# Kernel tuning notes

Hardware: AMD Instinct MI355X
Metric: run time of the kernel (lower is better)

## Reference

```python
import jax, jax.numpy as jnp
import numpy as np

B, L, D, V = 512, 128, 512, 100000

def setup_inputs() -> dict:
    key = jax.random.key(0)
    ks = jax.random.split(key, 8)
    return {
        "t1s": jax.random.randint(ks[0], (B,), 0, V),
        "t2s": jax.random.randint(ks[1], (B,), 0, V),
        "t1_contexts": jax.random.randint(ks[2], (B, L), 0, V),
        "t2_contexts": jax.random.randint(ks[3], (B, L), 0, V),
        "embed_table": jax.random.normal(ks[4], (V, D), dtype=jnp.float32),
        "att_mat": jax.random.normal(ks[5], (D, D), dtype=jnp.float32) * (6.0 / (D + D)) ** 0.5,
        "w_pred": jax.random.normal(ks[6], (D, 1), dtype=jnp.float32) * 0.02,
        "b_pred": jnp.zeros((1,), dtype=jnp.float32),
    }

def _frob_normalize(x):
    # torch.norm(mat, p=2) is the Frobenius norm of the whole (L, D) matrix
    n = jnp.sqrt(jnp.sum(x * x, axis=(1, 2), keepdims=True))
    return x / n

def reference(t1s, t2s, t1_contexts, t2_contexts, embed_table, att_mat, w_pred, b_pred):
    # dropout is identity in eval mode; t1s/t2s embeddings are unused in the
    # 'dynamic' branch (dead code in the original forward).
    A = _frob_normalize(embed_table[t1_contexts])  # (B, L, D)
    Bm = _frob_normalize(embed_table[t2_contexts])  # (B, L, D)
    # batched bilinear attention: tanh(A @ att_mat @ B^T)
    S = jnp.tanh(jnp.einsum('bld,de,bme->blm', A, att_mat, Bm))  # (B, L, L)
    rows = jax.nn.softmax(jnp.mean(S, axis=2), axis=1)  # (B, L)
    cols = jax.nn.softmax(jnp.mean(S, axis=1), axis=1)  # (B, L)
    newA = jnp.einsum('bld,bl->bd', A, rows)   # (B, D)
    newB = jnp.einsum('bld,bl->bd', Bm, cols)  # (B, D)
    logits = ((newA * newB) @ w_pred + b_pred).reshape(-1)  # (B,)
    return logits, S
```

## Files before the change

### kernel.cpp

```cpp
#include <hip/hip_runtime.h>
#include <hip/hip_bf16.h>
#include <stdint.h>

#define NB 512
#define NL 128
#define ND 512

typedef __bf16 bf16;
typedef __bf16 bf16x8 __attribute__((ext_vector_type(8)));
typedef float  f32x4  __attribute__((ext_vector_type(4)));

#define GLDS(src, dst) __builtin_amdgcn_global_load_lds( \
    (const __attribute__((address_space(1))) void*)(src), \
    (__attribute__((address_space(3))) void*)(dst), 16, 0, 0)

__global__ __launch_bounds__(256) void k_gather(const int* __restrict__ ctx1,
                                                const int* __restrict__ ctx2,
                                                const float* __restrict__ table,
                                                bf16* __restrict__ d1,
                                                bf16* __restrict__ d2,
                                                float* __restrict__ ss,
                                                const float* __restrict__ att,
                                                bf16* __restrict__ attT) {
    const int b = blockIdx.x, side = blockIdx.y, zc = blockIdx.z, t = threadIdx.x;
    if (side == 2) {
        int chunk = b * 8 + zc;
        if (chunk < 1024) {
            int i = chunk * 256 + t;
            int n = i >> 9, k = i & 511;
            attT[i] = (bf16)att[k * 512 + n];
        }
        return;
    }
    const int* __restrict__ ctx = side ? ctx2 : ctx1;
    bf16* __restrict__ dst = side ? d2 : d1;
    const int base = b * NL;
    const int dv = t & 127, lr = t >> 7;
    int idxs[8];
    #pragma unroll
    for (int i = 0; i < 8; ++i) idxs[i] = ctx[base + zc * 16 + i * 2 + lr];
    float acc = 0.f;
    #pragma unroll
    for (int i = 0; i < 8; ++i) {
        int l = zc * 16 + i * 2 + lr;
        f32x4 v = __builtin_nontemporal_load(
            (const f32x4*)table + (size_t)idxs[i] * (ND / 4) + dv);
        acc += v[0]*v[0] + v[1]*v[1] + v[2]*v[2] + v[3]*v[3];
        union { bf16 h[4]; uint2 u; } pk;
        pk.h[0] = (bf16)v[0]; pk.h[1] = (bf16)v[1];
        pk.h[2] = (bf16)v[2]; pk.h[3] = (bf16)v[3];
        *((uint2*)(dst + (size_t)(base + l) * ND) + dv) = pk.u;
    }
    for (int o = 32; o; o >>= 1) acc += __shfl_xor(acc, o);
    __shared__ float red[4];
    if ((t & 63) == 0) red[t >> 6] = acc;
    __syncthreads();
    if (t == 0) atomicAdd(&ss[side * NB + b], red[0] + red[1] + red[2] + red[3]);
}

__global__ __launch_bounds__(512, 4) void k_mega3(
        const bf16* __restrict__ Ab, const bf16* __restrict__ attT,
        const bf16* __restrict__ Bb, float* __restrict__ Sout,
        const float* __restrict__ ss, const float* __restrict__ w_pred,
        const float* __restrict__ b_pred, float* __restrict__ logits) {
    const int b = blockIdx.x, row0 = b * NL, tid = threadIdx.x;
    const int lane = tid & 63, w = tid >> 6;
    const int lm = lane & 15, quad = lane >> 4;
    const int wm = (w & 1) * 64;
    const int wn = (w >> 1) * 32;

    __shared__ __align__(16) char smem[69888];
    bf16* Tch = (bf16*)(smem + 32768);
    float* pA   = (float*)smem;
    float* pB   = (float*)(smem + 16384);
    float* red2 = (float*)(smem + 65600);
    float* rowb = (float*)(smem + 65664);
    float* colb = (float*)(smem + 67712);
    float* wrow = (float*)(smem + 68736);
    float* wcol = (float*)(smem + 69248);

    const int rT = tid >> 2, slT = tid & 3;
    const int csT = slT ^ ((rT >> 1) & 3);

    f32x4 accS[4][2] = {};

    for (int nc = 0; nc < 4; ++nc) {
        const bf16* attN = attT + (size_t)(nc * 128) * ND;
        f32x4 acc1[4][2] = {};

        GLDS(Ab + (size_t)(row0 + rT) * ND + csT * 8, (bf16*)smem + tid * 8);
        GLDS(attN + (size_t)rT * ND + csT * 8, (bf16*)(smem + 8192) + tid * 8);

        for (int t = 0; t < 16; ++t) {
            if (t < 15) {
                const int k0 = (t + 1) * 32, p = (t + 1) & 1;
                GLDS(Ab + (size_t)(row0 + rT) * ND + k0 + csT * 8,
                     (bf16*)(smem + p * 16384) + tid * 8);
                GLDS(attN + (size_t)rT * ND + k0 + csT * 8,
                     (bf16*)(smem + p * 16384 + 8192) + tid * 8);
                asm volatile("s_waitcnt vmcnt(2)" ::: "memory");
            } else {
                asm volatile("s_waitcnt vmcnt(0)" ::: "memory");
            }
            __builtin_amdgcn_s_barrier();
            const bf16* A_ = (bf16*)(smem + (t & 1) * 16384);
            const bf16* N_ = (bf16*)(smem + (t & 1) * 16384 + 8192);
            bf16x8 af[4], bf2[2];
            #pragma unroll
            for (int t4 = 0; t4 < 4; ++t4) {
                int R = wm + t4 * 16 + lm;
                af[t4] = *(const bf16x8*)&A_[R * 32 + (quad ^ ((R >> 1) & 3)) * 8];
            }
            #pragma unroll
            for (int t2 = 0; t2 < 2; ++t2) {
                int R = wn + t2 * 16 + lm;
                bf2[t2] = *(const bf16x8*)&N_[R * 32 + (quad ^ ((R >> 1) & 3)) * 8];
            }
            __builtin_amdgcn_s_setprio(1);
            #pragma unroll
            for (int im = 0; im < 4; ++im)
                #pragma unroll
                for (int jn = 0; jn < 2; ++jn)
                    acc1[im][jn] = __builtin_amdgcn_mfma_f32_16x16x32_bf16(
                        af[im], bf2[jn], acc1[im][jn], 0, 0, 0);
            __builtin_amdgcn_s_setprio(0);
            __builtin_amdgcn_s_barrier();
        }

        #pragma unroll
        for (int i = 0; i < 4; ++i)
            GLDS(Bb + (size_t)(row0 + rT) * ND + nc * 128 + i * 32 + csT * 8,
                 (bf16*)(smem + i * 8192) + tid * 8);
        #pragma unroll
        for (int im = 0; im < 4; ++im)
        #pragma unroll
        for (int jn = 0; jn < 2; ++jn)
        #pragma unroll
        for (int p = 0; p < 4; ++p) {
            int m = wm + im * 16 + quad * 4 + p;
            int n = wn + jn * 16 + lm;
            int ks = n >> 6, c = n & 63;
            int pos = (((c >> 3) ^ (m & 7)) << 3) + (c & 7);
            Tch[ks * 8192 + m * 64 + pos] = (bf16)acc1[im][jn][p];
        }
        __syncthreads();

        __builtin_amdgcn_s_setprio(1);
        #pragma unroll
        for (int th = 0; th < 2; ++th) {
            const bf16* Tk = Tch + th * 8192;
            #pragma unroll
            for (int kk = 0; kk < 2; ++kk) {
                const bf16* Bs_ = (bf16*)(smem + (th * 2 + kk) * 8192);
                const int ca = (kk * 4 + quad) ^ (lm & 7);
                bf16x8 af[4], bf2[2];
                #pragma unroll
                for (int t4 = 0; t4 < 4; ++t4)
                    af[t4] = *(const bf16x8*)&Tk[(wm + t4 * 16 + lm) * 64 + ca * 8];
                #pragma unroll
                for (int t2 = 0; t2 < 2; ++t2) {
                    int R = wn + t2 * 16 + lm;
                    bf2[t2] = *(const bf16x8*)&Bs_[R * 32 + (quad ^ ((R >> 1) & 3)) * 8];
                }
                #pragma unroll
                for (int im = 0; im < 4; ++im)
                    #pragma unroll
                    for (int jn = 0; jn < 2; ++jn)
                        accS[im][jn] = __builtin_amdgcn_mfma_f32_16x16x32_bf16(
                            af[im], bf2[jn], accS[im][jn], 0, 0, 0);
            }
        }
        __builtin_amdgcn_s_setprio(0);
        __syncthreads();
    }

    const float ssA = ss[b], ssB = ss[NB + b];
    const float sc = rsqrtf(ssA * ssB);
    float* __restrict__ Sb = Sout + (size_t)b * NL * NL;
    #pragma unroll
    for (int im = 0; im < 4; ++im)
    #pragma unroll
    for (int jn = 0; jn < 2; ++jn)
    #pragma unroll
    for (int p = 0; p < 4; ++p) {
        float v = tanhf(accS[im][jn][p] * sc);
        accS[im][jn][p] = v;
        int m = wm + im * 16 + quad * 4 + p;
        int n = wn + jn * 16 + lm;
        __builtin_nontemporal_store(v, &Sb[m * NL + n]);
    }
    #pragma unroll
    for (int im = 0; im < 4; ++im)
    #pragma unroll
    for (int p = 0; p < 4; ++p) {
        float r = accS[im][0][p] + accS[im][1][p];
        r += __shfl_xor(r, 1); r += __shfl_xor(r, 2);
        r += __shfl_xor(r, 4); r += __shfl_xor(r, 8);
        if (lm == 0) rowb[(w >> 1) * NL + wm + im * 16 + quad * 4 + p] = r;
    }
    #pragma unroll
    for (int jn = 0; jn < 2; ++jn) {
        float cv = 0.f;
        #pragma unroll
        for (int im = 0; im < 4; ++im)
            #pragma unroll
            for (int p = 0; p < 4; ++p) cv += accS[im][jn][p];
        cv += __shfl_xor(cv, 16); cv += __shfl_xor(cv, 32);
        if (quad == 0) colb[(w & 1) * NL + wn + jn * 16 + lm] = cv;
    }
    __syncthreads();

    if (tid < 64) {
        float a  = (rowb[tid] + rowb[NL + tid] + rowb[2 * NL + tid] + rowb[3 * NL + tid]) * (1.f / NL);
        float c2 = (rowb[tid + 64] + rowb[NL + tid + 64] + rowb[2 * NL + tid + 64] + rowb[3 * NL + tid + 64]) * (1.f / NL);
        float mx = fmaxf(a, c2);
        for (int o = 32; o; o >>= 1) mx = fmaxf(mx, __shfl_xor(mx, o));
        float e0 = expf(a - mx), e1 = expf(c2 - mx);
        float s = e0 + e1;
        for (int o = 32; o; o >>= 1) s += __shfl_xor(s, o);
        float inv = 1.f / s;
        wrow[tid] = e0 * inv; wrow[tid + 64] = e1 * inv;
    } else if (tid < 128) {
        int q = tid - 64;
        float a  = (colb[q] + colb[NL + q]) * (1.f / NL);
        float c2 = (colb[q + 64] + colb[NL + q + 64]) * (1.f / NL);
        float mx = fmaxf(a, c2);
        for (int o = 32; o; o >>= 1) mx = fmaxf(mx, __shfl_xor(mx, o));
        float e0 = expf(a - mx), e1 = expf(c2 - mx);
        float s = e0 + e1;
        for (int o = 32; o; o >>= 1) s += __shfl_xor(s, o);
        float inv = 1.f / s;
        wcol[q] = e0 * inv; wcol[q + 64] = e1 * inv;
    }
    __syncthreads();

    const int c = tid & 63, g = tid >> 6;
    const bf16* __restrict__ Abase = Ab + (size_t)b * NL * ND;
    const bf16* __restrict__ Bbase = Bb + (size_t)b * NL * ND;
    float aacc[8] = {}, bacc[8] = {};
    for (int l = g; l < NL; l += 8) {
        float wr = wrow[l], wc = wcol[l];
        bf16x8 va = *(const bf16x8*)(Abase + (size_t)l * ND + c * 8);
        bf16x8 vb = *(const bf16x8*)(Bbase + (size_t)l * ND + c * 8);
        #pragma unroll
        for (int j = 0; j < 8; ++j) {
            aacc[j] += wr * (float)va[j];
            bacc[j] += wc * (float)vb[j];
        }
    }
    #pragma unroll
    for (int j = 0; j < 8; ++j) {
        pA[g * ND + c * 8 + j] = aacc[j];
        pB[g * ND + c * 8 + j] = bacc[j];
    }
    __syncthreads();

    if (tid < 64) {
        float dot = 0.f;
        #pragma unroll
        for (int j = 0; j < 8; ++j) {
            int d = tid * 8 + j;
            float na = 0.f, nb = 0.f;
            #pragma unroll
            for (int g2 = 0; g2 < 8; ++g2) {
                na += pA[g2 * ND + d];
                nb += pB[g2 * ND + d];
            }
            dot += na * nb * w_pred[d];
        }
        for (int o = 32; o; o >>= 1) dot += __shfl_xor(dot, o);
        if (tid == 0)
            logits[b] = dot * rsqrtf(ssA) * rsqrtf(ssB) + b_pred[0];
    }
}

extern "C" void kernel_launch(void* const* d_in, const int* in_sizes, int n_in,
                              void* d_out, int out_size, void* d_ws, size_t ws_size,
                              hipStream_t stream) {
    const int*   t1c = (const int*)d_in[2];
    const int*   t2c = (const int*)d_in[3];
    const float* emb = (const float*)d_in[4];
    const float* att = (const float*)d_in[5];
    const float* wp  = (const float*)d_in[6];
    const float* bp  = (const float*)d_in[7];

    float* out    = (float*)d_out;
    float* logits = out;
    float* S      = out + NB;

    char* ws = (char*)d_ws;
    bf16*  Ab   = (bf16*)(ws);
    bf16*  Bb   = (bf16*)(ws + 67108864);
    bf16*  attT = (bf16*)(ws + 134217728);
    float* ss   = (float*)(ws + 134742016);

    hipMemsetAsync(ss, 0, 4096, stream);
    k_gather<<<dim3(NB, 3, 8), 256, 0, stream>>>(t1c, t2c, emb, Ab, Bb, ss, att, attT);
    k_mega3<<<dim3(NB), 512, 0, stream>>>(Ab, attT, Bb, S, ss, wp, bp, logits);
}
```

Measured before the change: 446.3 us.

## Restructure bilinear GEMM chain into two row halves with direct global fragment loads

Reworks the fused attention kernel. The old version staged A and att tiles through LDS with global_load_lds double buffering over four column chunks. The new version splits the 128 rows into two halves, and in each half every wave computes a 64x64 slab of A·att over the full K dimension. MFMA fragments are read straight from global memory without LDS staging. The intermediate T goes to LDS and is multiplied by B fragments, also loaded directly from global. This drops the LDS staging and barriers for the first GEMM, but risks lower global load efficiency and more redundant reads of A and att across waves, plus higher register pressure from the 4x4 accumulator tile.

```diff
diff --git a/kernel.cpp b/kernel.cpp
--- a/kernel.cpp
+++ b/kernel.cpp
@@ -9,10 +9,6 @@
 typedef __bf16 bf16;
 typedef __bf16 bf16x8 __attribute__((ext_vector_type(8)));
 typedef float  f32x4  __attribute__((ext_vector_type(4)));
-
-#define GLDS(src, dst) __builtin_amdgcn_global_load_lds( \
-    (const __attribute__((address_space(1))) void*)(src), \
-    (__attribute__((address_space(3))) void*)(dst), 16, 0, 0)
 
 __global__ __launch_bounds__(256) void k_gather(const int* __restrict__ ctx1,
                                                 const int* __restrict__ ctx2,
@@ -58,7 +54,7 @@
     if (t == 0) atomicAdd(&ss[side * NB + b], red[0] + red[1] + red[2] + red[3]);
 }
 
-__global__ __launch_bounds__(512, 4) void k_mega3(
+__global__ __launch_bounds__(512, 4) void k_mega4(
         const bf16* __restrict__ Ab, const bf16* __restrict__ attT,
         const bf16* __restrict__ Bb, float* __restrict__ Sout,
         const float* __restrict__ ss, const float* __restrict__ w_pred,
@@ -66,153 +62,114 @@
     const int b = blockIdx.x, row0 = b * NL, tid = threadIdx.x;
     const int lane = tid & 63, w = tid >> 6;
     const int lm = lane & 15, quad = lane >> 4;
-    const int wm = (w & 1) * 64;
-    const int wn = (w >> 1) * 32;
-
-    __shared__ __align__(16) char smem[69888];
-    bf16* Tch = (bf16*)(smem + 32768);
+    const int nb1 = w * 64;
+    const int nb2 = w * 16;
+
+    __shared__ __align__(16) char smem[69632];
+    bf16*  Tls  = (bf16*)smem;
+    float* rowp = (float*)smem;
     float* pA   = (float*)smem;
     float* pB   = (float*)(smem + 16384);
-    float* red2 = (float*)(smem + 65600);
-    float* rowb = (float*)(smem + 65664);
-    float* colb = (float*)(smem + 67712);
-    float* wrow = (float*)(smem + 68736);
-    float* wcol = (float*)(smem + 69248);
-
-    const int rT = tid >> 2, slT = tid & 3;
-    const int csT = slT ^ ((rT >> 1) & 3);
-
-    f32x4 accS[4][2] = {};
-
-    for (int nc = 0; nc < 4; ++nc) {
-        const bf16* attN = attT + (size_t)(nc * 128) * ND;
-        f32x4 acc1[4][2] = {};
-
-        GLDS(Ab + (size_t)(row0 + rT) * ND + csT * 8, (bf16*)smem + tid * 8);
-        GLDS(attN + (size_t)rT * ND + csT * 8, (bf16*)(smem + 8192) + tid * 8);
-
-        for (int t = 0; t < 16; ++t) {
-            if (t < 15) {
-                const int k0 = (t + 1) * 32, p = (t + 1) & 1;
-                GLDS(Ab + (size_t)(row0 + rT) * ND + k0 + csT * 8,
-                     (bf16*)(smem + p * 16384) + tid * 8);
-                GLDS(attN + (size_t)rT * ND + k0 + csT * 8,
-                     (bf16*)(smem + p * 16384 + 8192) + tid * 8);
-                asm volatile("s_waitcnt vmcnt(2)" ::: "memory");
-            } else {
-                asm volatile("s_waitcnt vmcnt(0)" ::: "memory");
-            }
-            __builtin_amdgcn_s_barrier();
-            const bf16* A_ = (bf16*)(smem + (t & 1) * 16384);
-            const bf16* N_ = (bf16*)(smem + (t & 1) * 16384 + 8192);
-            bf16x8 af[4], bf2[2];
-            #pragma unroll
-            for (int t4 = 0; t4 < 4; ++t4) {
-                int R = wm + t4 * 16 + lm;
-                af[t4] = *(const bf16x8*)&A_[R * 32 + (quad ^ ((R >> 1) & 3)) * 8];
-            }
-            #pragma unroll
-            for (int t2 = 0; t2 < 2; ++t2) {
-                int R = wn + t2 * 16 + lm;
-                bf2[t2] = *(const bf16x8*)&N_[R * 32 + (quad ^ ((R >> 1) & 3)) * 8];
-            }
-            __builtin_amdgcn_s_setprio(1);
-            #pragma unroll
-            for (int im = 0; im < 4; ++im)
-                #pragma unroll
-                for (int jn = 0; jn < 2; ++jn)
-                    acc1[im][jn] = __builtin_amdgcn_mfma_f32_16x16x32_bf16(
-                        af[im], bf2[jn], acc1[im][jn], 0, 0, 0);
-            __builtin_amdgcn_s_setprio(0);
-            __builtin_amdgcn_s_barrier();
-        }
-
-        #pragma unroll
-        for (int i = 0; i < 4; ++i)
-            GLDS(Bb + (size_t)(row0 + rT) * ND + nc * 128 + i * 32 + csT * 8,
-                 (bf16*)(smem + i * 8192) + tid * 8);
-        #pragma unroll
-        for (int im = 0; im < 4; ++im)
-        #pragma unroll
-        for (int jn = 0; jn < 2; ++jn)
-        #pragma unroll
-        for (int p = 0; p < 4; ++p) {
-            int m = wm + im * 16 + quad * 4 + p;
-            int n = wn + jn * 16 + lm;
-            int ks = n >> 6, c = n & 63;
-            int pos = (((c >> 3) ^ (m & 7)) << 3) + (c & 7);
-            Tch[ks * 8192 + m * 64 + pos] = (bf16)acc1[im][jn][p];
-        }
-        __syncthreads();
-
-        __builtin_amdgcn_s_setprio(1);
-        #pragma unroll
-        for (int th = 0; th < 2; ++th) {
-            const bf16* Tk = Tch + th * 8192;
-            #pragma unroll
-            for (int kk = 0; kk < 2; ++kk) {
-                const bf16* Bs_ = (bf16*)(smem + (th * 2 + kk) * 8192);
-                const int ca = (kk * 4 + quad) ^ (lm & 7);
-                bf16x8 af[4], bf2[2];
-                #pragma unroll
-                for (int t4 = 0; t4 < 4; ++t4)
-                    af[t4] = *(const bf16x8*)&Tk[(wm + t4 * 16 + lm) * 64 + ca * 8];
-                #pragma unroll
-                for (int t2 = 0; t2 < 2; ++t2) {
-                    int R = wn + t2 * 16 + lm;
-                    bf2[t2] = *(const bf16x8*)&Bs_[R * 32 + (quad ^ ((R >> 1) & 3)) * 8];
-                }
-                #pragma unroll
-                for (int im = 0; im < 4; ++im)
-                    #pragma unroll
-                    for (int jn = 0; jn < 2; ++jn)
-                        accS[im][jn] = __builtin_amdgcn_mfma_f32_16x16x32_bf16(
-                            af[im], bf2[jn], accS[im][jn], 0, 0, 0);
-            }
-        }
-        __builtin_amdgcn_s_setprio(0);
-        __syncthreads();
-    }
+    float* rowb = (float*)(smem + 65536);
+    float* colp = (float*)(smem + 66048);
+    float* wrow = (float*)(smem + 67072);
+    float* wcol = (float*)(smem + 67584);
 
     const float ssA = ss[b], ssB = ss[NB + b];
     const float sc = rsqrtf(ssA * ssB);
     float* __restrict__ Sb = Sout + (size_t)b * NL * NL;
-    #pragma unroll
-    for (int im = 0; im < 4; ++im)
-    #pragma unroll
-    for (int jn = 0; jn < 2; ++jn)
-    #pragma unroll
-    for (int p = 0; p < 4; ++p) {
-        float v = tanhf(accS[im][jn][p] * sc);
-        accS[im][jn][p] = v;
-        int m = wm + im * 16 + quad * 4 + p;
-        int n = wn + jn * 16 + lm;
-        __builtin_nontemporal_store(v, &Sb[m * NL + n]);
-    }
-    #pragma unroll
-    for (int im = 0; im < 4; ++im)
-    #pragma unroll
-    for (int p = 0; p < 4; ++p) {
-        float r = accS[im][0][p] + accS[im][1][p];
-        r += __shfl_xor(r, 1); r += __shfl_xor(r, 2);
-        r += __shfl_xor(r, 4); r += __shfl_xor(r, 8);
-        if (lm == 0) rowb[(w >> 1) * NL + wm + im * 16 + quad * 4 + p] = r;
-    }
-    #pragma unroll
-    for (int jn = 0; jn < 2; ++jn) {
-        float cv = 0.f;
-        #pragma unroll
-        for (int im = 0; im < 4; ++im)
-            #pragma unroll
-            for (int p = 0; p < 4; ++p) cv += accS[im][jn][p];
-        cv += __shfl_xor(cv, 16); cv += __shfl_xor(cv, 32);
-        if (quad == 0) colb[(w & 1) * NL + wn + jn * 16 + lm] = cv;
-    }
-    __syncthreads();
+
+    for (int h = 0; h < 2; ++h) {
+        const int m0 = h * 64;
+
+        f32x4 acc1[4][4] = {};
+        for (int t = 0; t < 16; ++t) {
+            const int k0 = t * 32 + quad * 8;
+            bf16x8 af[4], bfm[4];
+            #pragma unroll
+            for (int mf = 0; mf < 4; ++mf)
+                af[mf] = *(const bf16x8*)(Ab + (size_t)(row0 + m0 + mf * 16 + lm) * ND + k0);
+            #pragma unroll
+            for (int nf = 0; nf < 4; ++nf)
+                bfm[nf] = *(const bf16x8*)(attT + (size_t)(nb1 + nf * 16 + lm) * ND + k0);
+            #pragma unroll
+            for (int mf = 0; mf < 4; ++mf)
+                #pragma unroll
+                for (int nf = 0; nf < 4; ++nf)
+                    acc1[mf][nf] = __builtin_amdgcn_mfma_f32_16x16x32_bf16(
+                        af[mf], bfm[nf], acc1[mf][nf], 0, 0, 0);
+        }
+
+        #pragma unroll
+        for (int mf = 0; mf < 4; ++mf)
+        #pragma unroll
+        for (int nf = 0; nf < 4; ++nf)
+        #pragma unroll
+        for (int p = 0; p < 4; ++p) {
+            int m = mf * 16 + quad * 4 + p;
+            int n = nb1 + nf * 16 + lm;
+            int ti = n >> 5, kq = (n >> 3) & 3, e = n & 7;
+            int pos = kq ^ ((m >> 1) & 3);
+            Tls[ti * 2048 + m * 32 + pos * 8 + e] = (bf16)acc1[mf][nf][p];
+        }
+        __syncthreads();
+
+        f32x4 accS[4] = {};
+        for (int t = 0; t < 16; ++t) {
+            bf16x8 tf[4];
+            bf16x8 bf1 = *(const bf16x8*)(Bb + (size_t)(row0 + nb2 + lm) * ND + t * 32 + quad * 8);
+            #pragma unroll
+            for (int mf = 0; mf < 4; ++mf) {
+                int R = mf * 16 + lm;
+                tf[mf] = *(const bf16x8*)&Tls[t * 2048 + R * 32 + (quad ^ ((R >> 1) & 3)) * 8];
+            }
+            #pragma unroll
+            for (int mf = 0; mf < 4; ++mf)
+                accS[mf] = __builtin_amdgcn_mfma_f32_16x16x32_bf16(
+                    tf[mf], bf1, accS[mf], 0, 0, 0);
+        }
+        __syncthreads();
+
+        #pragma unroll
+        for (int mf = 0; mf < 4; ++mf)
+        #pragma unroll
+        for (int p = 0; p < 4; ++p) {
+            float v = tanhf(accS[mf][p] * sc);
+            accS[mf][p] = v;
+            int m = m0 + mf * 16 + quad * 4 + p;
+            __builtin_nontemporal_store(v, &Sb[m * NL + nb2 + lm]);
+        }
+        #pragma unroll
+        for (int mf = 0; mf < 4; ++mf)
+        #pragma unroll
+        for (int p = 0; p < 4; ++p) {
+            float r = accS[mf][p];
+            r += __shfl_xor(r, 1); r += __shfl_xor(r, 2);
+            r += __shfl_xor(r, 4); r += __shfl_xor(r, 8);
+            if (lm == 0) rowp[w * 64 + mf * 16 + quad * 4 + p] = r;
+        }
+        {
+            float cv = 0.f;
+            #pragma unroll
+            for (int mf = 0; mf < 4; ++mf)
+                #pragma unroll
+                for (int p = 0; p < 4; ++p) cv += accS[mf][p];
+            cv += __shfl_xor(cv, 16); cv += __shfl_xor(cv, 32);
+            if (quad == 0) colp[h * 128 + nb2 + lm] = cv;
+        }
+        __syncthreads();
+        if (tid < 64) {
+            float r = 0.f;
+            #pragma unroll
+            for (int i = 0; i < 8; ++i) r += rowp[i * 64 + tid];
+            rowb[m0 + tid] = r;
+        }
+        __syncthreads();
+    }
 
     if (tid < 64) {
-        float a  = (rowb[tid] + rowb[NL + tid] + rowb[2 * NL + tid] + rowb[3 * NL + tid]) * (1.f / NL);
-        float c2 = (rowb[tid + 64] + rowb[NL + tid + 64] + rowb[2 * NL + tid + 64] + rowb[3 * NL + tid + 64]) * (1.f / NL);
+        float a  = rowb[tid] * (1.f / NL);
+        float c2 = rowb[tid + 64] * (1.f / NL);
         float mx = fmaxf(a, c2);
         for (int o = 32; o; o >>= 1) mx = fmaxf(mx, __shfl_xor(mx, o));
         float e0 = expf(a - mx), e1 = expf(c2 - mx);
@@ -222,8 +179,8 @@
         wrow[tid] = e0 * inv; wrow[tid + 64] = e1 * inv;
     } else if (tid < 128) {
         int q = tid - 64;
-        float a  = (colb[q] + colb[NL + q]) * (1.f / NL);
-        float c2 = (colb[q + 64] + colb[NL + q + 64]) * (1.f / NL);
+        float a  = (colp[q] + colp[128 + q]) * (1.f / NL);
+        float c2 = (colp[q + 64] + colp[192 + q]) * (1.f / NL);
         float mx = fmaxf(a, c2);
         for (int o = 32; o; o >>= 1) mx = fmaxf(mx, __shfl_xor(mx, o));
         float e0 = expf(a - mx), e1 = expf(c2 - mx);
@@ -296,5 +253,5 @@
 
     hipMemsetAsync(ss, 0, 4096, stream);
     k_gather<<<dim3(NB, 3, 8), 256, 0, stream>>>(t1c, t2c, emb, Ab, Bb, ss, att, attT);
-    k_mega3<<<dim3(NB), 512, 0, stream>>>(Ab, attT, Bb, S, ss, wp, bp, logits);
+    k_mega4<<<dim3(NB), 512, 0, stream>>>(Ab, attT, Bb, S, ss, wp, bp, logits);
 }
```

Measured after the change: 715.8 us. 1.6x slower.
